# Performance work log

Measured on AMD Instinct MI355X. Metric: run time of the kernel, lower is better.

Reference implementation:

```python
import jax, jax.numpy as jnp
import numpy as np

B, L, E, H = 4, 4096, 1024, 16
HD = E // H
I = 4096  # intermediate_size = 4*E
RMS_EPS = 1e-6
ATTN_EPS = 1e-6
GATE_INIT = 0.1  # 0.1 + 0.05*layer_idx, layer_idx=0


def rmsnorm(x, w, eps=RMS_EPS):
    xf = x.astype(jnp.float32)
    var = jnp.mean(xf * xf, axis=-1, keepdims=True)
    return w * (xf * jax.lax.rsqrt(var + eps)).astype(x.dtype)


def rotate_half(x):
    d = x.shape[-1] // 2
    return jnp.concatenate([-x[..., d:], x[..., :d]], axis=-1)


def setup_inputs() -> dict:
    key = jax.random.key(0)
    ks = jax.random.split(key, 16)
    h = jax.random.normal(ks[0], (B, L, E), jnp.float32)
    c = jax.random.normal(ks[1], (B, E), jnp.float32)
    # standard RoPE tables, shape (L, HD)
    pos = jnp.arange(L, dtype=jnp.float32)
    inv = 1.0 / (10000.0 ** (jnp.arange(0, HD, 2, dtype=jnp.float32) / HD))
    fr = pos[:, None] * inv[None, :]
    emb = jnp.concatenate([fr, fr], axis=-1)
    cos, sin = jnp.cos(emb), jnp.sin(emb)
    s = 0.02
    Wq = jax.random.normal(ks[2], (E, E), jnp.float32) * s
    Wk = jax.random.normal(ks[3], (E, E), jnp.float32) * s
    Wv = jax.random.normal(ks[4], (E, E), jnp.float32) * s
    Wo = jax.random.normal(ks[5], (E, E), jnp.float32) * s
    Wg = jax.random.normal(ks[6], (I, E), jnp.float32) * s
    Wu = jax.random.normal(ks[7], (I, E), jnp.float32) * s
    Wd = jax.random.normal(ks[8], (E, I), jnp.float32) * s
    w_norm1 = jnp.ones((E,), jnp.float32)
    w_norm2 = jnp.ones((E,), jnp.float32)
    Wada = jax.random.normal(ks[9], (6 * E, E), jnp.float32) * 0.01
    bada = np.zeros((6 * E,), np.float32)
    bada[2 * E:3 * E] = GATE_INIT  # gate_msa
    bada[5 * E:6 * E] = GATE_INIT  # gate_mlp
    bada = jnp.asarray(bada)
    return {"h": h, "c": c, "cos": cos, "sin": sin, "Wq": Wq, "Wk": Wk,
            "Wv": Wv, "Wo": Wo, "Wg": Wg, "Wu": Wu, "Wd": Wd,
            "w_norm1": w_norm1, "w_norm2": w_norm2, "Wada": Wada, "bada": bada}


def reference(h, c, cos, sin, Wq, Wk, Wv, Wo, Wg, Wu, Wd, w_norm1, w_norm2, Wada, bada):
    # adaLN modulation: (B, 6E) -> six (B,1,E) chunks
    mod = c @ Wada.T + bada
    sh1, sc1, g1, sh2, sc2, g2 = [m[:, None, :] for m in jnp.split(mod, 6, axis=-1)]

    # --- attention branch ---
    x = rmsnorm(h, w_norm1) * (1.0 + sc1) + sh1  # modulate
    q = jax.nn.silu(x @ Wq.T).reshape(B, L, H, HD).transpose(0, 2, 1, 3)  # (B,H,L,hd)
    k = jax.nn.silu(x @ Wk.T).reshape(B, L, H, HD).transpose(0, 2, 1, 3)
    v = (x @ Wv.T).reshape(B, L, H, HD).transpose(0, 2, 1, 3)
    cs = cos[None, None]  # (1,1,L,hd)
    sn = sin[None, None]
    q = q * cs + rotate_half(q) * sn
    k = k * cs + rotate_half(k) * sn
    # cosFormer sin/cos feature map; m = max(src,tgt) = L
    idx = (np.pi / 2) * jnp.arange(1, L + 1, dtype=jnp.float32) / L  # (L,)
    sw = jnp.sin(idx)[None, None, :, None]
    cw = jnp.cos(idx)[None, None, :, None]
    q_ = jnp.concatenate([q * sw, q * cw], axis=-1)  # (B,H,L,2hd)
    k_ = jnp.concatenate([k * sw, k * cw], axis=-1)
    # non-causal linear attention: K^T V first (O(L))
    kv = jnp.einsum('bhld,bhlm->bhdm', k_, v)             # (B,H,2hd,hd)
    z = 1.0 / jnp.maximum(jnp.einsum('bhld,bhd->bhl', q_, k_.sum(axis=2)), ATTN_EPS)
    attn = jnp.einsum('bhld,bhdm,bhl->bhlm', q_, kv, z)   # (B,H,L,hd)
    attn = attn.transpose(0, 2, 1, 3).reshape(B, L, E) @ Wo.T
    h = h + g1 * attn  # bias_dropout_add_scale, eval mode

    # --- MLP branch ---
    x = rmsnorm(h, w_norm2) * (1.0 + sc2) + sh2
    mlp = (jax.nn.silu(x @ Wg.T) * (x @ Wu.T)) @ Wd.T
    return h + g2 * mlp
```

## Files before the change

### kernel.cpp

```cpp
#include <hip/hip_runtime.h>
#include <hip/hip_bf16.h>

#define BB 4
#define LL 4096
#define EE 1024
#define HH 16
#define II 4096
#define MM (BB*LL)

using f32x4 = __attribute__((ext_vector_type(4))) float;
using s16x8 = __attribute__((ext_vector_type(8))) short;
using u32x4 = __attribute__((ext_vector_type(4))) unsigned int;

__device__ __forceinline__ unsigned short f2bf(float f) {
  union { float f; unsigned u; } x; x.f = f;
  unsigned r = x.u + 0x7fffu + ((x.u >> 16) & 1u);
  return (unsigned short)(r >> 16);
}
__device__ __forceinline__ float bf2f(unsigned short s) {
  union { unsigned u; float f; } x; x.u = ((unsigned)s) << 16;
  return x.f;
}
__device__ __forceinline__ float silu_f(float x) { return x / (1.0f + expf(-x)); }

__device__ __forceinline__ void gll16(const void* g, void* l) {
  __builtin_amdgcn_global_load_lds(
      (const __attribute__((address_space(1))) unsigned int*)g,
      (__attribute__((address_space(3))) unsigned int*)l, 16, 0, 0);
}

__global__ __launch_bounds__(256) void k_mod(const float* __restrict__ c,
    const float* __restrict__ Wada, const float* __restrict__ bada,
    float* __restrict__ mod) {
  __shared__ float cs[EE];
  int b = blockIdx.y;
  int n = blockIdx.x * 256 + threadIdx.x;
  for (int i = threadIdx.x; i < EE; i += 256) cs[i] = c[b*EE + i];
  __syncthreads();
  const float4* wp = (const float4*)(Wada + (size_t)n * EE);
  float acc = 0.f;
  for (int k = 0; k < EE/4; k++) {
    float4 t = wp[k];
    acc += t.x*cs[4*k] + t.y*cs[4*k+1] + t.z*cs[4*k+2] + t.w*cs[4*k+3];
  }
  mod[(size_t)b*6*EE + n] = acc + bada[n];
}

__global__ __launch_bounds__(256) void k_coef(const float* __restrict__ mod,
    const float* __restrict__ w1, const float* __restrict__ w2,
    float* __restrict__ cf1, float* __restrict__ cf2) {
  int k = blockIdx.x * 256 + threadIdx.x;
  int b = blockIdx.y;
  const float* mb = mod + (size_t)b*6*EE;
  cf1[(size_t)b*2048 + k]        = w1[k] * (1.0f + mb[EE + k]);
  cf1[(size_t)b*2048 + 1024 + k] = mb[k];
  cf2[(size_t)b*2048 + k]        = w2[k] * (1.0f + mb[4*EE + k]);
  cf2[(size_t)b*2048 + 1024 + k] = mb[3*EE + k];
}

__global__ __launch_bounds__(256) void k_rsig(const float* __restrict__ in,
    float* __restrict__ rsig) {
  int row = blockIdx.x;
  int t = threadIdx.x;
  float4 v = ((const float4*)(in + (size_t)row * EE))[t];
  float ss = v.x*v.x + v.y*v.y + v.z*v.z + v.w*v.w;
  #pragma unroll
  for (int o = 32; o > 0; o >>= 1) ss += __shfl_down(ss, o, 64);
  __shared__ float red[4];
  if ((t & 63) == 0) red[t >> 6] = ss;
  __syncthreads();
  float tot = red[0] + red[1] + red[2] + red[3];
  if (t == 0) rsig[row] = 1.0f / sqrtf(tot * (1.0f/1024.0f) + 1e-6f);
}

__global__ __launch_bounds__(256) void k_f2b(const float* __restrict__ s,
    unsigned short* __restrict__ d, int n4) {
  int i = blockIdx.x * 256 + threadIdx.x;
  if (i >= n4) return;
  float4 v = ((const float4*)s)[i];
  ushort4 u; u.x = f2bf(v.x); u.y = f2bf(v.y); u.z = f2bf(v.z); u.w = f2bf(v.w);
  ((ushort4*)d)[i] = u;
}

__global__ __launch_bounds__(256) void k_split1(const float* __restrict__ h,
    const float* __restrict__ rsig, const float* __restrict__ cf,
    unsigned short* __restrict__ xh, unsigned short* __restrict__ xl) {
  int row = blockIdx.x;
  int t = threadIdx.x;
  int b = row >> 12;
  float rs = rsig[row];
  const float* cfb = cf + (size_t)b*2048;
  float4 v  = ((const float4*)(h + (size_t)row*EE))[t];
  float4 c1 = ((const float4*)cfb)[t];
  float4 c0 = ((const float4*)(cfb + 1024))[t];
  float x0 = fmaf(v.x*rs, c1.x, c0.x);
  float x1 = fmaf(v.y*rs, c1.y, c0.y);
  float x2 = fmaf(v.z*rs, c1.z, c0.z);
  float x3 = fmaf(v.w*rs, c1.w, c0.w);
  ushort4 uh, ul;
  uh.x = f2bf(x0); ul.x = f2bf(x0 - bf2f(uh.x));
  uh.y = f2bf(x1); ul.y = f2bf(x1 - bf2f(uh.y));
  uh.z = f2bf(x2); ul.z = f2bf(x2 - bf2f(uh.z));
  uh.w = f2bf(x3); ul.w = f2bf(x3 - bf2f(uh.w));
  ((ushort4*)(xh + (size_t)row*EE))[t] = uh;
  ((ushort4*)(xl + (size_t)row*EE))[t] = ul;
}

__global__ __launch_bounds__(256) void k_split2(const float* __restrict__ in,
    const float* __restrict__ rsig, const float* __restrict__ cf,
    unsigned short* __restrict__ xb) {
  int row = blockIdx.x;
  int t = threadIdx.x;
  int b = row >> 12;
  float rs = rsig[row];
  const float* cfb = cf + (size_t)b*2048;
  float4 v  = ((const float4*)(in + (size_t)row*EE))[t];
  float4 c1 = ((const float4*)cfb)[t];
  float4 c0 = ((const float4*)(cfb + 1024))[t];
  ushort4 u;
  u.x = f2bf(fmaf(v.x*rs, c1.x, c0.x));
  u.y = f2bf(fmaf(v.y*rs, c1.y, c0.y));
  u.z = f2bf(fmaf(v.z*rs, c1.z, c0.z));
  u.w = f2bf(fmaf(v.w*rs, c1.w, c0.w));
  ((ushort4*)(xb + (size_t)row*EE))[t] = u;
}

__global__ __launch_bounds__(256) void k_sgemmK(
    const float* __restrict__ Ah, const float* __restrict__ W,
    const float* __restrict__ rsig, const float* __restrict__ cf,
    const float* __restrict__ cosT, const float* __restrict__ sinT,
    float* __restrict__ outq) {
  __shared__ float As[8][128];
  __shared__ float Bs[8][128];
  __shared__ float c1s[1024];
  __shared__ float c0s[1024];
  int t = threadIdx.x;
  int tx = t & 15, ty = t >> 4;
  int bm = blockIdx.x, bn = blockIdx.y;
  int srow = t >> 1, sk = (t & 1) * 4;
  int bidx = bm >> 5;
  for (int i = t; i < 1024; i += 256) {
    c1s[i] = cf[(size_t)bidx*2048 + i];
    c0s[i] = cf[(size_t)bidx*2048 + 1024 + i];
  }
  int arow = bm*128 + srow;
  float rsA = rsig[arow];
  const float* ap = Ah + (size_t)arow*EE + sk;
  const float* bp = W + (size_t)(bn*128 + srow)*EE + sk;
  float acc[8][8];
  #pragma unroll
  for (int i = 0; i < 8; i++)
    #pragma unroll
    for (int j = 0; j < 8; j++) acc[i][j] = 0.f;
  float4 pa = *(const float4*)ap;
  float4 pb = *(const float4*)bp;
  int c0 = (tx < 8) ? tx*4 : 64 + (tx - 8)*4;
  __syncthreads();
  for (int k0 = 0; k0 < EE; k0 += 8) {
    int kb = k0 + sk;
    As[sk+0][srow] = fmaf(pa.x*rsA, c1s[kb+0], c0s[kb+0]);
    As[sk+1][srow] = fmaf(pa.y*rsA, c1s[kb+1], c0s[kb+1]);
    As[sk+2][srow] = fmaf(pa.z*rsA, c1s[kb+2], c0s[kb+2]);
    As[sk+3][srow] = fmaf(pa.w*rsA, c1s[kb+3], c0s[kb+3]);
    Bs[sk+0][srow] = pb.x; Bs[sk+1][srow] = pb.y; Bs[sk+2][srow] = pb.z; Bs[sk+3][srow] = pb.w;
    __syncthreads();
    if (k0 + 8 < EE) {
      pa = *(const float4*)(ap + k0 + 8);
      pb = *(const float4*)(bp + k0 + 8);
    }
    #pragma unroll
    for (int k = 0; k < 8; k++) {
      float4 a0 = *(const float4*)&As[k][ty*8];
      float4 a1 = *(const float4*)&As[k][ty*8+4];
      float4 b0 = *(const float4*)&Bs[k][c0];
      float4 b1 = *(const float4*)&Bs[k][c0+32];
      float av[8] = {a0.x,a0.y,a0.z,a0.w,a1.x,a1.y,a1.z,a1.w};
      float bv[8]  = {b0.x,b0.y,b0.z,b0.w,b1.x,b1.y,b1.z,b1.w};
      #pragma unroll
      for (int i = 0; i < 8; i++)
        #pragma unroll
        for (int j = 0; j < 8; j++)
          acc[i][j] = fmaf(av[i], bv[j], acc[i][j]);
    }
    __syncthreads();
  }
  int head = bn*2 + (tx >= 8 ? 1 : 0);
  int d0 = (tx < 8) ? tx*4 : (tx - 8)*4;
  #pragma unroll
  for (int i = 0; i < 8; i++) {
    int m = bm*128 + ty*8 + i;
    int b = m >> 12, l = m & 4095;
    const float* cp = cosT + (size_t)l*64;
    const float* sp = sinT + (size_t)l*64;
    float4 cl  = *(const float4*)(cp + d0);
    float4 slv = *(const float4*)(sp + d0);
    float4 chv = *(const float4*)(cp + d0 + 32);
    float4 shv = *(const float4*)(sp + d0 + 32);
    float sA0 = silu_f(acc[i][0]), sA1 = silu_f(acc[i][1]), sA2 = silu_f(acc[i][2]), sA3 = silu_f(acc[i][3]);
    float sB0 = silu_f(acc[i][4]), sB1 = silu_f(acc[i][5]), sB2 = silu_f(acc[i][6]), sB3 = silu_f(acc[i][7]);
    float q00 = sA0*cl.x - sB0*slv.x;
    float q01 = sA1*cl.y - sB1*slv.y;
    float q02 = sA2*cl.z - sB2*slv.z;
    float q03 = sA3*cl.w - sB3*slv.w;
    float q10 = sB0*chv.x + sA0*shv.x;
    float q11 = sB1*chv.y + sA1*shv.y;
    float q12 = sB2*chv.z + sA2*shv.z;
    float q13 = sB3*chv.w + sA3*shv.w;
    float* op = outq + ((size_t)(b*HH + head)*LL + l)*64;
    *(float4*)(op + d0)      = make_float4(q00, q01, q02, q03);
    *(float4*)(op + d0 + 32) = make_float4(q10, q11, q12, q13);
  }
}

__global__ __launch_bounds__(256) void k_qk(
    const unsigned short* __restrict__ xh, const unsigned short* __restrict__ xl,
    const float* __restrict__ W,
    const float* __restrict__ cosT, const float* __restrict__ sinT,
    float* __restrict__ outq) {
  __shared__ unsigned short Ah[128*32];
  __shared__ unsigned short Al[128*32];
  __shared__ unsigned short Bh[64*40];
  __shared__ unsigned short Bl[64*40];
  int t = threadIdx.x, w = t >> 6, lane = t & 63;
  int bm = blockIdx.x, bn = blockIdx.y;
  int wm = (w & 1) * 64;
  int wn = (w >> 1) * 16;
  int r16 = lane & 15, kg = lane >> 4;
  int rin = lane >> 2, slot = lane & 3;
  int ar0 = w*32 + rin, ar1 = ar0 + 16;
  const unsigned short* ahg0 = xh + (size_t)(bm*128 + ar0)*EE + (size_t)((((ar0>>1)&3) ^ slot) * 8);
  const unsigned short* ahg1 = xh + (size_t)(bm*128 + ar1)*EE + (size_t)((((ar1>>1)&3) ^ slot) * 8);
  const unsigned short* alg0 = xl + (size_t)(bm*128 + ar0)*EE + (size_t)((((ar0>>1)&3) ^ slot) * 8);
  const unsigned short* alg1 = xl + (size_t)(bm*128 + ar1)*EE + (size_t)((((ar1>>1)&3) ^ slot) * 8);
  unsigned short* ahl0 = &Ah[(w*32 + 0) * 32];
  unsigned short* ahl1 = &Ah[(w*32 + 16) * 32];
  unsigned short* all0 = &Al[(w*32 + 0) * 32];
  unsigned short* all1 = &Al[(w*32 + 16) * 32];
  int srow = t >> 2, koff = (t & 3) * 8;
  const float* bp = W + (size_t)(bn*64 + srow)*EE + koff;
  float4 pb0 = *(const float4*)(bp + 0);
  float4 pb1 = *(const float4*)(bp + 4);
  f32x4 acc[4][2];
  #pragma unroll
  for (int i = 0; i < 4; i++) { acc[i][0] = (f32x4){0,0,0,0}; acc[i][1] = (f32x4){0,0,0,0}; }

  for (int k0 = 0; k0 < EE; k0 += 32) {
    gll16(ahg0 + k0, ahl0);
    gll16(ahg1 + k0, ahl1);
    gll16(alg0 + k0, all0);
    gll16(alg1 + k0, all1);
    {
      unsigned short h0 = f2bf(pb0.x), h1 = f2bf(pb0.y), h2 = f2bf(pb0.z), h3 = f2bf(pb0.w);
      unsigned short h4 = f2bf(pb1.x), h5 = f2bf(pb1.y), h6 = f2bf(pb1.z), h7 = f2bf(pb1.w);
      unsigned short l0 = f2bf(pb0.x - bf2f(h0)), l1 = f2bf(pb0.y - bf2f(h1));
      unsigned short l2 = f2bf(pb0.z - bf2f(h2)), l3 = f2bf(pb0.w - bf2f(h3));
      unsigned short l4 = f2bf(pb1.x - bf2f(h4)), l5 = f2bf(pb1.y - bf2f(h5));
      unsigned short l6 = f2bf(pb1.z - bf2f(h6)), l7 = f2bf(pb1.w - bf2f(h7));
      u32x4 uh, ul;
      uh[0] = ((unsigned)h1<<16)|h0; uh[1] = ((unsigned)h3<<16)|h2;
      uh[2] = ((unsigned)h5<<16)|h4; uh[3] = ((unsigned)h7<<16)|h6;
      ul[0] = ((unsigned)l1<<16)|l0; ul[1] = ((unsigned)l3<<16)|l2;
      ul[2] = ((unsigned)l5<<16)|l4; ul[3] = ((unsigned)l7<<16)|l6;
      *(u32x4*)&Bh[srow*40 + koff] = uh;
      *(u32x4*)&Bl[srow*40 + koff] = ul;
    }
    __syncthreads();
    if (k0 + 32 < EE) {
      pb0 = *(const float4*)(bp + k0 + 32);
      pb1 = *(const float4*)(bp + k0 + 36);
    }
    int brow0 = wn + r16, brow1 = wn + 32 + r16;
    s16x8 bh0 = *(const s16x8*)&Bh[brow0*40 + kg*8];
    s16x8 bl0 = *(const s16x8*)&Bl[brow0*40 + kg*8];
    s16x8 bh1 = *(const s16x8*)&Bh[brow1*40 + kg*8];
    s16x8 bl1 = *(const s16x8*)&Bl[brow1*40 + kg*8];
    #pragma unroll
    for (int i = 0; i < 4; i++) {
      int row = wm + i*16 + r16;
      int sw = ((((row>>1)&3) ^ kg) << 3);
      s16x8 ah = *(const s16x8*)&Ah[row*32 + sw];
      s16x8 al = *(const s16x8*)&Al[row*32 + sw];
      acc[i][0] = __builtin_amdgcn_mfma_f32_16x16x32_bf16(ah, bh0, acc[i][0], 0, 0, 0);
      acc[i][0] = __builtin_amdgcn_mfma_f32_16x16x32_bf16(ah, bl0, acc[i][0], 0, 0, 0);
      acc[i][0] = __builtin_amdgcn_mfma_f32_16x16x32_bf16(al, bh0, acc[i][0], 0, 0, 0);
      acc[i][1] = __builtin_amdgcn_mfma_f32_16x16x32_bf16(ah, bh1, acc[i][1], 0, 0, 0);
      acc[i][1] = __builtin_amdgcn_mfma_f32_16x16x32_bf16(ah, bl1, acc[i][1], 0, 0, 0);
      acc[i][1] = __builtin_amdgcn_mfma_f32_16x16x32_bf16(al, bh1, acc[i][1], 0, 0, 0);
    }
    __syncthreads();
  }
  int d = wn + r16;
  #pragma unroll
  for (int i = 0; i < 4; i++) {
    #pragma unroll
    for (int r = 0; r < 4; r++) {
      int mm = bm*128 + wm + i*16 + kg*4 + r;
      int b = mm >> 12, l = mm & 4095;
      const float* cp = cosT + (size_t)l*64;
      const float* sp = sinT + (size_t)l*64;
      float sl = silu_f(acc[i][0][r]);
      float sh = silu_f(acc[i][1][r]);
      float qlo = sl*cp[d]      - sh*sp[d];
      float qhi = sh*cp[d + 32] + sl*sp[d + 32];
      float* op = outq + (((size_t)(b*HH + bn))*LL + l)*64;
      op[d]      = qlo;
      op[d + 32] = qhi;
    }
  }
}

template<int EPI, int KLEN, int SA, int SB>
__global__ __launch_bounds__(256) void k_gemm2(
    const unsigned short* __restrict__ Ab,
    const unsigned short* __restrict__ Bw,
    int kbB, int bnoff,
    const float* __restrict__ res, const float* __restrict__ mod,
    unsigned short* __restrict__ outb, float* __restrict__ outf) {
  __shared__ unsigned short As[128 * 32];
  __shared__ unsigned short Bs[128 * 32];
  int t = threadIdx.x, w = t >> 6, lane = t & 63;
  int bm = blockIdx.x, bn = blockIdx.y;
  int wm = (w >> 1) * 64, wn = (w & 1) * 64;
  int rin = lane >> 2, slot = lane & 3;
  int brow0 = w*32 + rin, brow1 = brow0 + 16;
  int swz0 = (((brow0>>1)&3) ^ slot) * 8;
  int swz1 = (((brow1>>1)&3) ^ slot) * 8;
  const unsigned short* ag0 = Ab + (size_t)(bm*128 + brow0)*SA + swz0;
  const unsigned short* ag1 = Ab + (size_t)(bm*128 + brow1)*SA + swz1;
  const unsigned short* bg0 = Bw + (size_t)(bnoff + bn*128 + brow0)*SB + kbB + swz0;
  const unsigned short* bg1 = Bw + (size_t)(bnoff + bn*128 + brow1)*SB + kbB + swz1;
  unsigned short* al0 = &As[(w*32 + 0) * 32];
  unsigned short* al1 = &As[(w*32 + 16) * 32];
  unsigned short* bl0 = &Bs[(w*32 + 0) * 32];
  unsigned short* bl1 = &Bs[(w*32 + 16) * 32];
  f32x4 acc[4][4];
  #pragma unroll
  for (int i = 0; i < 4; i++)
    #pragma unroll
    for (int j = 0; j < 4; j++) acc[i][j] = (f32x4){0.f, 0.f, 0.f, 0.f};
  int r16 = lane & 15, kg = lane >> 4;
  for (int k0 = 0; k0 < KLEN; k0 += 32) {
    gll16(ag0 + k0, al0);
    gll16(ag1 + k0, al1);
    gll16(bg0 + k0, bl0);
    gll16(bg1 + k0, bl1);
    __syncthreads();
    s16x8 af[4], bfr[4];
    #pragma unroll
    for (int i = 0; i < 4; i++) {
      int row = wm + i*16 + r16;
      af[i] = *(const s16x8*)&As[row*32 + ((((row>>1)&3) ^ kg) << 3)];
    }
    #pragma unroll
    for (int j = 0; j < 4; j++) {
      int row = wn + j*16 + r16;
      bfr[j] = *(const s16x8*)&Bs[row*32 + ((((row>>1)&3) ^ kg) << 3)];
    }
    #pragma unroll
    for (int i = 0; i < 4; i++)
      #pragma unroll
      for (int j = 0; j < 4; j++)
        acc[i][j] = __builtin_amdgcn_mfma_f32_16x16x32_bf16(af[i], bfr[j], acc[i][j], 0, 0, 0);
    __syncthreads();
  }
  #pragma unroll
  for (int i = 0; i < 4; i++) {
    #pragma unroll
    for (int j = 0; j < 4; j++) {
      int nn = bn*128 + wn + j*16 + r16;
      #pragma unroll
      for (int r = 0; r < 4; r++) {
        int mm = bm*128 + wm + i*16 + kg*4 + r;
        float v = acc[i][j][r];
        if constexpr (EPI == 0) {
          int b = mm >> 12, l = mm & 4095, hh = nn >> 6, dd = nn & 63;
          outb[(((size_t)(b*HH + hh))*LL + l)*64 + dd] = f2bf(v);
        } else if constexpr (EPI == 1) {
          int b = mm >> 12;
          size_t o = (size_t)mm*EE + nn;
          outf[o] = res[o] + mod[(size_t)b*6*EE + 2*EE + nn] * v;
        } else if constexpr (EPI == 2) {
          outb[(size_t)mm*2048 + nn] = f2bf(silu_f(v));
        } else if constexpr (EPI == 3) {
          size_t o = (size_t)mm*2048 + nn;
          outb[o] = f2bf(bf2f(outb[o]) * v);
        } else {
          int b = mm >> 12;
          size_t o = (size_t)mm*EE + nn;
          outf[o] = res[o] + mod[(size_t)b*6*EE + 5*EE + nn] * v;
        }
      }
    }
  }
}

__global__ __launch_bounds__(256) void k_kvpart(const float* __restrict__ kr,
    const unsigned short* __restrict__ vtb, float* __restrict__ kvp) {
  int bi = blockIdx.x;
  int bh = bi >> 3, ch = bi & 7;
  const float* kp = kr + ((size_t)bh*LL + ch*512)*64;
  const unsigned short* vp = vtb + ((size_t)bh*LL + ch*512)*64;
  __shared__ float k8[8][64];
  __shared__ float v8[8][64];
  __shared__ float sw8[8], cw8[8];
  int t = threadIdx.x;
  int d = t >> 2, mq = (t & 3) * 16;
  float accS[16], accC[16];
  #pragma unroll
  for (int q = 0; q < 16; q++) { accS[q] = 0.f; accC[q] = 0.f; }
  float ksS = 0.f, ksC = 0.f;
  for (int l0 = 0; l0 < 512; l0 += 8) {
    __syncthreads();
    #pragma unroll
    for (int rep = 0; rep < 2; rep++) {
      int idx = rep*256 + t;
      k8[idx>>6][idx&63] = kp[(size_t)(l0 + (idx>>6))*64 + (idx&63)];
      v8[idx>>6][idx&63] = bf2f(vp[(size_t)(l0 + (idx>>6))*64 + (idx&63)]);
    }
    if (t < 8) {
      int gl = ch*512 + l0 + t;
      float idxv = 1.5707964f * (float)(gl + 1) * (1.0f/4096.0f);
      sw8[t] = sinf(idxv);
      cw8[t] = cosf(idxv);
    }
    __syncthreads();
    #pragma unroll
    for (int l = 0; l < 8; l++) {
      float kd = k8[l][d];
      float s = kd * sw8[l];
      float c = kd * cw8[l];
      ksS += s; ksC += c;
      const float4* vv = (const float4*)&v8[l][mq];
      #pragma unroll
      for (int q = 0; q < 4; q++) {
        float4 x = vv[q];
        accS[4*q+0] = fmaf(s, x.x, accS[4*q+0]);
        accS[4*q+1] = fmaf(s, x.y, accS[4*q+1]);
        accS[4*q+2] = fmaf(s, x.z, accS[4*q+2]);
        accS[4*q+3] = fmaf(s, x.w, accS[4*q+3]);
        accC[4*q+0] = fmaf(c, x.x, accC[4*q+0]);
        accC[4*q+1] = fmaf(c, x.y, accC[4*q+1]);
        accC[4*q+2] = fmaf(c, x.z, accC[4*q+2]);
        accC[4*q+3] = fmaf(c, x.w, accC[4*q+3]);
      }
    }
  }
  float* op = kvp + (size_t)bi * 8320;
  #pragma unroll
  for (int q = 0; q < 16; q++) {
    op[d*64 + mq + q]        = accS[q];
    op[4096 + d*64 + mq + q] = accC[q];
  }
  if (mq == 0) { op[8192 + d] = ksS; op[8256 + d] = ksC; }
}

__global__ __launch_bounds__(256) void k_kvred(const float* __restrict__ kvp,
    float* __restrict__ kvb) {
  int bh = blockIdx.x;
  for (int i = threadIdx.x; i < 8320; i += 256) {
    float s = 0.f;
    #pragma unroll
    for (int c = 0; c < 8; c++) s += kvp[((size_t)bh*8 + c)*8320 + i];
    kvb[(size_t)bh*8320 + i] = s;
  }
}

__global__ void k_zero(int* __restrict__ cnt) { if (threadIdx.x == 0) *cnt = 0; }

__global__ __launch_bounds__(256) void k_z(const float* __restrict__ qr,
    const float* __restrict__ kvb, float* __restrict__ zb,
    int* __restrict__ list, int* __restrict__ cnt) {
  int bh = blockIdx.x >> 6, lc = blockIdx.x & 63;
  __shared__ float ksS_s[64], ksC_s[64];
  int t = threadIdx.x;
  if (t < 64) ksS_s[t] = kvb[(size_t)bh*8320 + 8192 + t];
  else if (t < 128) ksC_s[t-64] = kvb[(size_t)bh*8320 + 8256 + (t-64)];
  __syncthreads();
  int l = lc*64 + (t >> 2), part = t & 3;
  const float4* qp = (const float4*)(qr + ((size_t)bh*LL + l)*64 + part*16);
  float A = 0.f, Bv = 0.f;
  #pragma unroll
  for (int q = 0; q < 4; q++) {
    float4 x = qp[q];
    int kb = part*16 + 4*q;
    A  += x.x*ksS_s[kb] + x.y*ksS_s[kb+1] + x.z*ksS_s[kb+2] + x.w*ksS_s[kb+3];
    Bv += x.x*ksC_s[kb] + x.y*ksC_s[kb+1] + x.z*ksC_s[kb+2] + x.w*ksC_s[kb+3];
  }
  A  += __shfl_xor(A, 1, 64);  A  += __shfl_xor(A, 2, 64);
  Bv += __shfl_xor(Bv, 1, 64); Bv += __shfl_xor(Bv, 2, 64);
  if (part == 0) {
    float idxv = 1.5707964f * (float)(l + 1) * (1.0f/4096.0f);
    float denom = sinf(idxv)*A + cosf(idxv)*Bv;
    int gid = bh*LL + l;
    zb[gid] = 1.0f / fmaxf(denom, 1e-6f);
    if (fabsf(denom) < 0.05f) {
      int idx = atomicAdd(cnt, 1);
      list[idx] = gid;
    }
  }
}

__global__ __launch_bounds__(256) void k_zfix(const float* __restrict__ h,
    const float* __restrict__ rsig, const float* __restrict__ cf,
    const float* __restrict__ Wq,
    const float* __restrict__ cosT, const float* __restrict__ sinT,
    const float* __restrict__ kvb, const int* __restrict__ list,
    const int* __restrict__ cnt, float* __restrict__ zb) {
  __shared__ float xs[1024];
  __shared__ double qd[64];
  __shared__ double sq[64];
  int n = *cnt;
  int t = threadIdx.x;
  for (int i = blockIdx.x; i < n; i += gridDim.x) {
    int gid = list[i];
    int bh = gid >> 12, l = gid & 4095;
    int b = bh >> 4, hh = bh & 15;
    int row = b*4096 + l;
    float rs = rsig[row];
    const float* cfb = cf + (size_t)b*2048;
    for (int k = t; k < 1024; k += 256)
      xs[k] = fmaf(h[(size_t)row*1024 + k]*rs, cfb[k], cfb[1024 + k]);
    __syncthreads();
    int j = t >> 2, s = t & 3;
    const float* wrow = Wq + (size_t)(hh*64 + j)*1024 + s*256;
    double acc = 0.0;
    for (int k = 0; k < 256; k++)
      acc += (double)wrow[k] * (double)xs[s*256 + k];
    acc += __shfl_xor(acc, 1, 64);
    acc += __shfl_xor(acc, 2, 64);
    if (s == 0) qd[j] = acc;
    __syncthreads();
    if (t < 64) {
      double qv = qd[t];
      sq[t] = qv / (1.0 + exp(-qv));
    }
    __syncthreads();
    if (t == 0) {
      const float* cp = cosT + (size_t)l*64;
      const float* sp = sinT + (size_t)l*64;
      const float* ksS = kvb + (size_t)bh*8320 + 8192;
      const float* ksC = kvb + (size_t)bh*8320 + 8256;
      double dS = 0.0, dC = 0.0;
      for (int d = 0; d < 64; d++) {
        double rot = (d < 32) ? -sq[d + 32] : sq[d - 32];
        double qe = sq[d]*(double)cp[d] + rot*(double)sp[d];
        dS += qe * (double)ksS[d];
        dC += qe * (double)ksC[d];
      }
      double idxv = 1.5707963267948966 * (double)(l + 1) / 4096.0;
      float denom = (float)(sin(idxv)*dS + cos(idxv)*dC);
      zb[gid] = 1.0f / fmaxf(denom, 1e-6f);
    }
    __syncthreads();
  }
}

__global__ __launch_bounds__(256) void k_attn(const float* __restrict__ qr,
    const float* __restrict__ kvb, const float* __restrict__ zb,
    unsigned short* __restrict__ attnb) {
  int bh = blockIdx.x >> 4, lc = blockIdx.x & 15;
  int t = threadIdx.x, w = t >> 6, lane = t & 63;
  const float* kvp_ = kvb + (size_t)bh*8320;
  float kvS[64], kvC[64];
  #pragma unroll
  for (int d = 0; d < 64; d++) kvS[d] = kvp_[d*64 + lane];
  #pragma unroll
  for (int d = 0; d < 64; d++) kvC[d] = kvp_[4096 + d*64 + lane];
  int b = bh >> 4, hh = bh & 15;
  int lbase = lc*256 + w*64;
  for (int li = 0; li < 64; li++) {
    int l = lbase + li;
    const float* qp = qr + ((size_t)bh*LL + l)*64;
    float qv = qp[lane];
    float z = zb[(size_t)bh*LL + l];
    float a0 = 0.f, a1 = 0.f, a2 = 0.f, a3 = 0.f;
    float b0 = 0.f, b1 = 0.f, b2 = 0.f, b3 = 0.f;
    #pragma unroll
    for (int d = 0; d < 64; d += 4) {
      float q0 = __uint_as_float(__builtin_amdgcn_readlane(__float_as_uint(qv), d+0));
      float q1 = __uint_as_float(__builtin_amdgcn_readlane(__float_as_uint(qv), d+1));
      float q2 = __uint_as_float(__builtin_amdgcn_readlane(__float_as_uint(qv), d+2));
      float q3 = __uint_as_float(__builtin_amdgcn_readlane(__float_as_uint(qv), d+3));
      a0 = fmaf(q0, kvS[d+0], a0);
      a1 = fmaf(q1, kvS[d+1], a1);
      a2 = fmaf(q2, kvS[d+2], a2);
      a3 = fmaf(q3, kvS[d+3], a3);
      b0 = fmaf(q0, kvC[d+0], b0);
      b1 = fmaf(q1, kvC[d+1], b1);
      b2 = fmaf(q2, kvC[d+2], b2);
      b3 = fmaf(q3, kvC[d+3], b3);
    }
    float A = (a0 + a1) + (a2 + a3);
    float Bv = (b0 + b1) + (b2 + b3);
    float idxv = 1.5707964f * (float)(l + 1) * (1.0f/4096.0f);
    float num = sinf(idxv)*A + cosf(idxv)*Bv;
    attnb[(((size_t)b*LL + l)*HH + hh)*64 + lane] = f2bf(num * z);
  }
}

extern "C" void kernel_launch(void* const* d_in, const int* in_sizes, int n_in,
                              void* d_out, int out_size, void* d_ws, size_t ws_size,
                              hipStream_t stream) {
  const float* h    = (const float*)d_in[0];
  const float* c    = (const float*)d_in[1];
  const float* cosT = (const float*)d_in[2];
  const float* sinT = (const float*)d_in[3];
  const float* Wq   = (const float*)d_in[4];
  const float* Wk   = (const float*)d_in[5];
  const float* Wv   = (const float*)d_in[6];
  const float* Wo   = (const float*)d_in[7];
  const float* Wg   = (const float*)d_in[8];
  const float* Wu   = (const float*)d_in[9];
  const float* Wd   = (const float*)d_in[10];
  const float* w1   = (const float*)d_in[11];
  const float* w2   = (const float*)d_in[12];
  const float* Wada = (const float*)d_in[13];
  const float* bada = (const float*)d_in[14];
  float* out = (float*)d_out;

  constexpr size_t BIG_SZ   = (size_t)MM * II * 2;
  constexpr size_t WS_NEEDED = BIG_SZ + 131072 + 32768*2 + 65536*2
      + 1048576 + 2129920 + 2097152*2 + 8388608*3;
  if (ws_size < WS_NEEDED) return;

  char* p = (char*)d_ws;
  char* big = p;                               p += BIG_SZ;
  float* mod = (float*)p;                      p += 131072;
  float* cf1 = (float*)p;                      p += 32768;
  float* cf2 = (float*)p;                      p += 32768;
  float* rsig1 = (float*)p;                    p += 65536;
  float* rsig2 = (float*)p;                    p += 65536;
  float* zb  = (float*)p;                      p += 1048576;
  float* kvb = (float*)p;                      p += 2129920;
  unsigned short* Wvb = (unsigned short*)p;    p += 2097152;
  unsigned short* Wob = (unsigned short*)p;    p += 2097152;
  unsigned short* Wgb = (unsigned short*)p;    p += 8388608;
  unsigned short* Wub = (unsigned short*)p;    p += 8388608;
  unsigned short* Wdb = (unsigned short*)p;    p += 8388608;
  unsigned short* xh   = (unsigned short*)big;
  unsigned short* xl   = (unsigned short*)(big + 33554432);
  unsigned short* vtb  = (unsigned short*)(big + 67108864);
  float* kvp           = (float*)(big + 100663296);
  float* qr            = (float*)(big + 67108864);
  int* zf_cnt          = (int*)big;
  int* zf_list         = (int*)(big + 256);
  unsigned short* attnb= (unsigned short*)big;
  unsigned short* x2b  = (unsigned short*)big;
  unsigned short* Pb   = (unsigned short*)(big + 33554432);
  float* kr            = (float*)d_out;

  k_mod<<<dim3(24, BB), 256, 0, stream>>>(c, Wada, bada, mod);
  k_coef<<<dim3(4, BB), 256, 0, stream>>>(mod, w1, w2, cf1, cf2);
  k_rsig<<<MM, 256, 0, stream>>>(h, rsig1);
  k_f2b<<<1024, 256, 0, stream>>>(Wv, Wvb, EE*EE/4);
  k_f2b<<<1024, 256, 0, stream>>>(Wo, Wob, EE*EE/4);
  k_f2b<<<4096, 256, 0, stream>>>(Wg, Wgb, II*EE/4);
  k_f2b<<<4096, 256, 0, stream>>>(Wu, Wub, II*EE/4);
  k_f2b<<<4096, 256, 0, stream>>>(Wd, Wdb, EE*II/4);
  k_split1<<<MM, 256, 0, stream>>>(h, rsig1, cf1, xh, xl);

  k_sgemmK<<<dim3(128, 8), 256, 0, stream>>>(h, Wk, rsig1, cf1, cosT, sinT, kr);
  k_gemm2<0, EE, EE, EE><<<dim3(128, 8), 256, 0, stream>>>(
      xh, Wvb, 0, 0, nullptr, nullptr, vtb, nullptr);
  k_kvpart<<<BB*HH*8, 256, 0, stream>>>(kr, vtb, kvp);
  k_kvred<<<BB*HH, 256, 0, stream>>>(kvp, kvb);

  k_qk<<<dim3(128, 16), 256, 0, stream>>>(xh, xl, Wq, cosT, sinT, qr);
  k_zero<<<1, 64, 0, stream>>>(zf_cnt);
  k_z<<<BB*HH*(LL/64), 256, 0, stream>>>(qr, kvb, zb, zf_list, zf_cnt);
  k_zfix<<<120, 256, 0, stream>>>(h, rsig1, cf1, Wq, cosT, sinT, kvb,
                                  zf_list, zf_cnt, zb);
  k_attn<<<BB*HH*(LL/256), 256, 0, stream>>>(qr, kvb, zb, attnb);

  k_gemm2<1, EE, EE, EE><<<dim3(128, 8), 256, 0, stream>>>(
      attnb, Wob, 0, 0, h, mod, nullptr, out);

  k_rsig<<<MM, 256, 0, stream>>>(out, rsig2);
  k_split2<<<MM, 256, 0, stream>>>(out, rsig2, cf2, x2b);
  for (int half = 0; half < 2; half++) {
    k_gemm2<2, EE, EE, EE><<<dim3(128, 16), 256, 0, stream>>>(
        x2b, Wgb, 0, half*2048, nullptr, nullptr, Pb, nullptr);
    k_gemm2<3, EE, EE, EE><<<dim3(128, 16), 256, 0, stream>>>(
        x2b, Wub, 0, half*2048, nullptr, nullptr, Pb, nullptr);
    k_gemm2<4, 2048, 2048, II><<<dim3(128, 8), 256, 0, stream>>>(
        Pb, Wdb, half*2048, 0, out, mod, nullptr, out);
  }
}
```

Before: 1.769 ms.

## Merge K and Q projection GEMMs into one role-dispatched kernel launch

The fp32 SGEMM for K and the split-bf16 MFMA GEMM for Q are now a single kernel whose blocks are interleaved 1:2 by role, with shared memory carved from one buffer. The aim is to let the two independent GEMMs share the GPU and fill each other's tail, and to drop a launch. The counter zeroing moves into k_kvred, and workspace buffers are re-laid out so that qr, vtb and kvp can all be live together. The cost is higher LDS and register use per block, taken as the maximum of the two roles, which may lower occupancy for the K role.

```diff
diff --git a/kernel.cpp b/kernel.cpp
--- a/kernel.cpp
+++ b/kernel.cpp
@@ -125,18 +125,17 @@
   ((ushort4*)(xb + (size_t)row*EE))[t] = u;
 }
 
-__global__ __launch_bounds__(256) void k_sgemmK(
+__device__ void role_sgemmK(char* smem, int bm, int bn,
     const float* __restrict__ Ah, const float* __restrict__ W,
     const float* __restrict__ rsig, const float* __restrict__ cf,
     const float* __restrict__ cosT, const float* __restrict__ sinT,
     float* __restrict__ outq) {
-  __shared__ float As[8][128];
-  __shared__ float Bs[8][128];
-  __shared__ float c1s[1024];
-  __shared__ float c0s[1024];
+  float (*As)[128] = (float(*)[128])(smem);
+  float (*Bs)[128] = (float(*)[128])(smem + 4096);
+  float* c1s = (float*)(smem + 8192);
+  float* c0s = (float*)(smem + 12288);
   int t = threadIdx.x;
   int tx = t & 15, ty = t >> 4;
-  int bm = blockIdx.x, bn = blockIdx.y;
   int srow = t >> 1, sk = (t & 1) * 4;
   int bidx = bm >> 5;
   for (int i = t; i < 1024; i += 256) {
@@ -212,17 +211,16 @@
   }
 }
 
-__global__ __launch_bounds__(256) void k_qk(
+__device__ void role_qk(char* smem, int bm, int bn,
     const unsigned short* __restrict__ xh, const unsigned short* __restrict__ xl,
     const float* __restrict__ W,
     const float* __restrict__ cosT, const float* __restrict__ sinT,
     float* __restrict__ outq) {
-  __shared__ unsigned short Ah[128*32];
-  __shared__ unsigned short Al[128*32];
-  __shared__ unsigned short Bh[64*40];
-  __shared__ unsigned short Bl[64*40];
+  unsigned short* Ah = (unsigned short*)smem;
+  unsigned short* Al = (unsigned short*)(smem + 8192);
+  unsigned short* Bh = (unsigned short*)(smem + 16384);
+  unsigned short* Bl = (unsigned short*)(smem + 21504);
   int t = threadIdx.x, w = t >> 6, lane = t & 63;
-  int bm = blockIdx.x, bn = blockIdx.y;
   int wm = (w & 1) * 64;
   int wn = (w >> 1) * 16;
   int r16 = lane & 15, kg = lane >> 4;
@@ -306,6 +304,25 @@
       op[d]      = qlo;
       op[d + 32] = qhi;
     }
+  }
+}
+
+__global__ __launch_bounds__(256) void k_megaKQ(
+    const float* __restrict__ h, const float* __restrict__ Wk,
+    const float* __restrict__ rsig, const float* __restrict__ cf,
+    const float* __restrict__ cosT, const float* __restrict__ sinT,
+    float* __restrict__ kr,
+    const unsigned short* __restrict__ xh, const unsigned short* __restrict__ xl,
+    const float* __restrict__ Wq, float* __restrict__ qr) {
+  __shared__ __align__(16) char smem[26624];
+  int bid = blockIdx.x;
+  int role = bid % 3;
+  int idx = bid / 3;
+  if (role == 0) {
+    role_sgemmK(smem, idx & 127, idx >> 7, h, Wk, rsig, cf, cosT, sinT, kr);
+  } else {
+    int qidx = idx*2 + (role - 1);
+    role_qk(smem, qidx & 127, qidx >> 7, xh, xl, Wq, cosT, sinT, qr);
   }
 }
 
@@ -455,8 +472,9 @@
 }
 
 __global__ __launch_bounds__(256) void k_kvred(const float* __restrict__ kvp,
-    float* __restrict__ kvb) {
+    float* __restrict__ kvb, int* __restrict__ cnt) {
   int bh = blockIdx.x;
+  if (bh == 0 && threadIdx.x == 0) *cnt = 0;
   for (int i = threadIdx.x; i < 8320; i += 256) {
     float s = 0.f;
     #pragma unroll
@@ -464,8 +482,6 @@
     kvb[(size_t)bh*8320 + i] = s;
   }
 }
-
-__global__ void k_zero(int* __restrict__ cnt) { if (threadIdx.x == 0) *cnt = 0; }
 
 __global__ __launch_bounds__(256) void k_z(const float* __restrict__ qr,
     const float* __restrict__ kvb, float* __restrict__ zb,
@@ -639,12 +655,12 @@
   unsigned short* Wdb = (unsigned short*)p;    p += 8388608;
   unsigned short* xh   = (unsigned short*)big;
   unsigned short* xl   = (unsigned short*)(big + 33554432);
-  unsigned short* vtb  = (unsigned short*)(big + 67108864);
-  float* kvp           = (float*)(big + 100663296);
   float* qr            = (float*)(big + 67108864);
-  int* zf_cnt          = (int*)big;
-  int* zf_list         = (int*)(big + 256);
-  unsigned short* attnb= (unsigned short*)big;
+  unsigned short* vtb  = (unsigned short*)(big + 33554432);
+  float* kvp           = (float*)big;
+  int* zf_cnt          = (int*)(big + 25165824);
+  int* zf_list         = (int*)(big + 25165824 + 256);
+  unsigned short* attnb= (unsigned short*)(big + 33554432);
   unsigned short* x2b  = (unsigned short*)big;
   unsigned short* Pb   = (unsigned short*)(big + 33554432);
   float* kr            = (float*)d_out;
@@ -659,14 +675,14 @@
   k_f2b<<<4096, 256, 0, stream>>>(Wd, Wdb, EE*II/4);
   k_split1<<<MM, 256, 0, stream>>>(h, rsig1, cf1, xh, xl);
 
-  k_sgemmK<<<dim3(128, 8), 256, 0, stream>>>(h, Wk, rsig1, cf1, cosT, sinT, kr);
+  k_megaKQ<<<3072, 256, 0, stream>>>(h, Wk, rsig1, cf1, cosT, sinT, kr,
+                                     xh, xl, Wq, qr);
+
   k_gemm2<0, EE, EE, EE><<<dim3(128, 8), 256, 0, stream>>>(
       xh, Wvb, 0, 0, nullptr, nullptr, vtb, nullptr);
+
   k_kvpart<<<BB*HH*8, 256, 0, stream>>>(kr, vtb, kvp);
-  k_kvred<<<BB*HH, 256, 0, stream>>>(kvp, kvb);
-
-  k_qk<<<dim3(128, 16), 256, 0, stream>>>(xh, xl, Wq, cosT, sinT, qr);
-  k_zero<<<1, 64, 0, stream>>>(zf_cnt);
+  k_kvred<<<BB*HH, 256, 0, stream>>>(kvp, kvb, zf_cnt);
   k_z<<<BB*HH*(LL/64), 256, 0, stream>>>(qr, kvb, zb, zf_list, zf_cnt);
   k_zfix<<<120, 256, 0, stream>>>(h, rsig1, cf1, Wq, cosT, sinT, kvb,
                                   zf_list, zf_cnt, zb);
```

Result: slower. 1.858 ms (+5.0%).
